# Kernel optimization log

Measured on AMD Instinct MI355X. Metric: run time of the kernel, lower is better.

The kernel has to match this reference:

```python
import jax, jax.numpy as jnp
import numpy as np

B, S, E, H, L = 16, 1024, 512, 8, 4
D = E // H  # head_dim = 64


def setup_inputs() -> dict:
    key = jax.random.key(0)
    ks = jax.random.split(key, 16)
    std = 0.02
    inp = {
        "q": jax.random.normal(ks[0], (B, S, E), jnp.float32),
        "k": jax.random.normal(ks[1], (B, S, E), jnp.float32),
        "v": jax.random.normal(ks[2], (B, S, E), jnp.float32),
        # standard Linear params (torch convention: W is (out, in))
        "Wq": jax.random.normal(ks[3], (E, E), jnp.float32) * std,
        "bq": jnp.zeros((E,), jnp.float32),
        "Wk": jax.random.normal(ks[4], (E, E), jnp.float32) * std,
        "bk": jnp.zeros((E,), jnp.float32),
        # WFLinear: shared weight elementwise-multiplied by per-language factor
        "Wv_share": jax.random.normal(ks[5], (E, E), jnp.float32) * std,
        "Wv_spec": 1.0 + jax.random.normal(ks[6], (L, E, E), jnp.float32) * std,
        "bv_share": jnp.zeros((E,), jnp.float32),
        "bv_spec": jax.random.normal(ks[7], (L, E), jnp.float32) * std,
        "Wo_share": jax.random.normal(ks[8], (E, E), jnp.float32) * std,
        "Wo_spec": 1.0 + jax.random.normal(ks[9], (L, E, E), jnp.float32) * std,
        "bo_share": jnp.zeros((E,), jnp.float32),
        "bo_spec": jax.random.normal(ks[10], (L, E), jnp.float32) * std,
        "mask": jax.random.randint(ks[11], (B, S), 0, 2, jnp.int32),
        "languageID": 1,
    }
    return inp


def reference(q, k, v, Wq, bq, Wk, bk, Wv_share, Wv_spec, bv_share, bv_spec,
              Wo_share, Wo_spec, bo_share, bo_spec, mask, languageID):
    scaling = D ** (-0.5)
    # projections (torch Linear: x @ W.T + b)
    Q = (q @ Wq.T + bq).reshape(B, S, H, D).transpose(0, 2, 1, 3) * scaling
    K = (k @ Wk.T + bk).reshape(B, S, H, D).transpose(0, 2, 1, 3)
    Wv = Wv_share * Wv_spec[languageID]
    bv = bv_share + bv_spec[languageID]
    V = (v @ Wv.T + bv).reshape(B, S, H, D).transpose(0, 2, 1, 3)
    # NOTE: faithful to original — Q already scaled by d_k^-0.5, and
    # AttentionWF divides by sqrt(d_k) AGAIN (effective scale 1/d_k).
    alpha = jnp.einsum("bhqd,bhkd->bhqk", Q, K) / np.float32(np.sqrt(D))
    m = (mask == 0)[:, None, None, :]  # (B,1,1,S) over key axis
    alpha = jnp.where(m, jnp.float32(-1e9), alpha)
    alpha = jax.nn.softmax(alpha, axis=-1)
    # dropout p=0.0 -> identity
    ctx = jnp.einsum("bhqk,bhkd->bhqd", alpha, V)  # (B,H,S,D)
    concat = ctx.transpose(0, 2, 1, 3).reshape(B, S, E)
    Wo = Wo_share * Wo_spec[languageID]
    bo = bo_share + bo_spec[languageID]
    return concat @ Wo.T + bo
```

## Files before the change

kernel.cpp:

```cpp
#include <hip/hip_runtime.h>

#define B_ 16
#define S_ 1024
#define E_ 512
#define H_ 8
#define D_ 64
#define L_ 4
#define M_ (B_*S_)

typedef unsigned short u16;
typedef __attribute__((ext_vector_type(8))) short bf16x8;
typedef __attribute__((ext_vector_type(4))) float f32x4;
typedef __attribute__((ext_vector_type(16))) float f32x16;
typedef __attribute__((ext_vector_type(4))) unsigned uint4v;
typedef __attribute__((ext_vector_type(2))) int int2v;

__device__ __forceinline__ u16 f2bf(float x) {
  unsigned u = __float_as_uint(x);
  unsigned r = (u + 0x7fffu + ((u >> 16) & 1u)) >> 16;
  return (u16)r;
}
__device__ __forceinline__ ushort4 f2bf4(float4 f) {
  ushort4 u;
  u.x = f2bf(f.x); u.y = f2bf(f.y); u.z = f2bf(f.z); u.w = f2bf(f.w);
  return u;
}
__device__ __forceinline__ unsigned cvt_pk_bf16(float lo, float hi) {
  unsigned r;
  asm("v_cvt_pk_bf16_f32 %0, %1, %2" : "=v"(r) : "v"(lo), "v"(hi));
  return r;
}
__device__ __forceinline__ int2v plswap(unsigned x, unsigned y) {
  return __builtin_amdgcn_permlane32_swap((int)x, (int)y, false, false);
}

typedef __attribute__((address_space(1))) const void gconst_void;
typedef __attribute__((address_space(3))) void lds_void;
__device__ __forceinline__ void gl_lds16(const void* g, void* l) {
  __builtin_amdgcn_global_load_lds((gconst_void*)g, (lds_void*)l, 16, 0, 0);
}
__device__ __forceinline__ void fence_vm0_barrier() {
  asm volatile("s_waitcnt vmcnt(0)" ::: "memory");
  __builtin_amdgcn_s_barrier();
}

__global__ __launch_bounds__(256) void prep_w(
    const float* __restrict__ Wq, const float* __restrict__ Wk,
    const float* __restrict__ Wv_sh, const float* __restrict__ Wv_sp,
    const float* __restrict__ Wo_sh, const float* __restrict__ Wo_sp,
    const float* __restrict__ bv_sh, const float* __restrict__ bv_sp,
    const float* __restrict__ bo_sh, const float* __restrict__ bo_sp,
    const int* __restrict__ langp,
    u16* __restrict__ Wq_b, u16* __restrict__ Wk_b,
    u16* __restrict__ Wv_b, u16* __restrict__ Wo_b,
    float* __restrict__ bv_f, float* __restrict__ bo_f) {
  int lang = langp[0];
  int i = blockIdx.x * 256 + threadIdx.x;
  size_t wofs = (size_t)lang * (E_*E_/4) + i;
  ((ushort4*)Wq_b)[i] = f2bf4(((const float4*)Wq)[i]);
  ((ushort4*)Wk_b)[i] = f2bf4(((const float4*)Wk)[i]);
  float4 vs = ((const float4*)Wv_sh)[i], vp = ((const float4*)Wv_sp)[wofs];
  float4 os = ((const float4*)Wo_sh)[i], op = ((const float4*)Wo_sp)[wofs];
  float4 vv = {vs.x*vp.x, vs.y*vp.y, vs.z*vp.z, vs.w*vp.w};
  float4 oo = {os.x*op.x, os.y*op.y, os.z*op.z, os.w*op.w};
  ((ushort4*)Wv_b)[i] = f2bf4(vv);
  ((ushort4*)Wo_b)[i] = f2bf4(oo);
  if (i < E_/4) {
    float4 b1 = ((const float4*)bv_sh)[i], b2 = ((const float4*)(bv_sp + (size_t)lang*E_))[i];
    float4 b3 = ((const float4*)bo_sh)[i], b4 = ((const float4*)(bo_sp + (size_t)lang*E_))[i];
    float4 r1 = {b1.x+b2.x, b1.y+b2.y, b1.z+b2.z, b1.w+b2.w};
    float4 r2 = {b3.x+b4.x, b3.y+b4.y, b3.z+b4.z, b3.w+b4.w};
    ((float4*)bv_f)[i] = r1;
    ((float4*)bo_f)[i] = r2;
  }
}

#define ABBUF 8192
__global__ __launch_bounds__(256, 4) void gemm_qkv(
    const float* __restrict__ q, const float* __restrict__ k, const float* __restrict__ v,
    const u16* __restrict__ Wq_b, const u16* __restrict__ Wk_b, const u16* __restrict__ Wv_b,
    const float* __restrict__ bq, const float* __restrict__ bk, const float* __restrict__ bv,
    u16* __restrict__ Qb, u16* __restrict__ Kb, u16* __restrict__ Vt) {
  __shared__ __align__(16) u16 sA[2*4096];
  __shared__ __align__(16) u16 sB[2*4096];
  const int z = blockIdx.y;
  const float* A    = (z == 0) ? q : (z == 1) ? k : v;
  const u16*   Bw   = (z == 0) ? Wq_b : (z == 1) ? Wk_b : Wv_b;
  const float* bias = (z == 0) ? bq : (z == 1) ? bk : bv;
  const int t = threadIdx.x;
  const int hw = blockIdx.x;
  const int wk = (hw & 7) * 64 + (hw >> 3);
  const int m0 = (wk >> 2) * 128, n0 = (wk & 3) * 128;
  const int lane = t & 63, wid = t >> 6;
  const int m16 = lane & 15, qq = lane >> 4;
  const int wrow = (wid >> 1) * 64, wcol = (wid & 1) * 64;
  const int key = (lane & 7) << 4;
  f32x4 acc[4][4] = {};
  const int arow = t >> 1;
  const float* aR = A + (size_t)(m0 + arow) * E_ + (t & 1) * 16;
  const int awr0 = (arow*64 + (t&1)*32)      ^ ((arow & 7) << 4);
  const int awr1 = (arow*64 + (t&1)*32 + 16) ^ ((arow & 7) << 4);
  const int cb0 = wid*2, cb1 = wid*2 + 1;
  const int rl0 = ((lane>>2)&1) ^ ((lane>>4)&1);
  const int brow = 2*(lane>>3) + rl0;
  const int bcol = (((lane&1)^rl0)<<3) + ((((lane>>1)&1) ^ ((lane>>3)&1))<<4);
  const u16* bp0 = Bw + (size_t)(n0 + cb0*16 + brow) * E_ + bcol;
  const u16* bp1 = Bw + (size_t)(n0 + cb1*16 + brow) * E_ + bcol;
  char* sAb = (char*)sA;
  char* sBb = (char*)sB;
  gl_lds16(bp0, sBb + cb0*1024);
  gl_lds16(bp1, sBb + cb1*1024);
  f32x4 ar0 = *(const f32x4*)aR;
  f32x4 ar1 = *(const f32x4*)(aR + 4);
  f32x4 ar2 = *(const f32x4*)(aR + 8);
  f32x4 ar3 = *(const f32x4*)(aR + 12);
  aR += 32; bp0 += 32; bp1 += 32;
  asm volatile("s_waitcnt vmcnt(0)" ::: "memory");
  {
    uint4v w0 = { cvt_pk_bf16(ar0[0],ar0[1]), cvt_pk_bf16(ar0[2],ar0[3]),
                  cvt_pk_bf16(ar1[0],ar1[1]), cvt_pk_bf16(ar1[2],ar1[3]) };
    uint4v w1 = { cvt_pk_bf16(ar2[0],ar2[1]), cvt_pk_bf16(ar2[2],ar2[3]),
                  cvt_pk_bf16(ar3[0],ar3[1]), cvt_pk_bf16(ar3[2],ar3[3]) };
    *(uint4v*)(sAb + awr0) = w0;
    *(uint4v*)(sAb + awr1) = w1;
  }
  asm volatile("s_waitcnt lgkmcnt(0)" ::: "memory");
  __builtin_amdgcn_s_barrier();
  for (int kt = 0; kt < 16; ++kt) {
    const int cur = (kt & 1) * ABBUF;
    const int nxt = ABBUF - cur;
    if (kt < 15) {
      gl_lds16(bp0, sBb + nxt + cb0*1024);
      gl_lds16(bp1, sBb + nxt + cb1*1024);
      ar0 = *(const f32x4*)aR;
      ar1 = *(const f32x4*)(aR + 4);
      ar2 = *(const f32x4*)(aR + 8);
      ar3 = *(const f32x4*)(aR + 12);
      aR += 32; bp0 += 32; bp1 += 32;
    }
    bf16x8 af[4], bfm[4];
#pragma unroll
    for (int mt = 0; mt < 4; ++mt) {
      int row = wrow + mt*16 + m16;
      af[mt] = *(const bf16x8*)(sAb + cur + ((row*64 + qq*16) ^ key));
    }
#pragma unroll
    for (int nt = 0; nt < 4; ++nt) {
      int row = wcol + nt*16 + m16;
      bfm[nt] = *(const bf16x8*)(sBb + cur + ((row*64 + qq*16) ^ key));
    }
#pragma unroll
    for (int mt = 0; mt < 4; ++mt)
#pragma unroll
      for (int nt = 0; nt < 4; ++nt)
        acc[mt][nt] = __builtin_amdgcn_mfma_f32_16x16x32_bf16(af[mt], bfm[nt], acc[mt][nt], 0, 0, 0);
    if (kt < 15) {
      asm volatile("s_waitcnt vmcnt(0)" ::: "memory");
      uint4v w0 = { cvt_pk_bf16(ar0[0],ar0[1]), cvt_pk_bf16(ar0[2],ar0[3]),
                    cvt_pk_bf16(ar1[0],ar1[1]), cvt_pk_bf16(ar1[2],ar1[3]) };
      uint4v w1 = { cvt_pk_bf16(ar2[0],ar2[1]), cvt_pk_bf16(ar2[2],ar2[3]),
                    cvt_pk_bf16(ar3[0],ar3[1]), cvt_pk_bf16(ar3[2],ar3[3]) };
      *(uint4v*)(sAb + nxt + awr0) = w0;
      *(uint4v*)(sAb + nxt + awr1) = w1;
      asm volatile("s_waitcnt lgkmcnt(0)" ::: "memory");
      __builtin_amdgcn_s_barrier();
    }
  }
  float bvv[4];
#pragma unroll
  for (int nt = 0; nt < 4; ++nt) bvv[nt] = bias[n0 + wcol + nt*16 + m16];
  if (z < 2) {
    u16* out = (z == 0) ? Qb : Kb;
#pragma unroll
    for (int mt = 0; mt < 4; ++mt) {
      int gm = m0 + wrow + mt*16 + qq*4;
#pragma unroll
      for (int nt = 0; nt < 4; ++nt) {
        int gn = n0 + wcol + nt*16 + m16;
#pragma unroll
        for (int r = 0; r < 4; ++r)
          out[(size_t)(gm + r) * E_ + gn] = f2bf(acc[mt][nt][r] + bvv[nt]);
      }
    }
  } else {
#pragma unroll
    for (int mt = 0; mt < 4; ++mt) {
      int tok0 = m0 + wrow + mt*16 + qq*4;
      int bb = tok0 >> 10, s0 = tok0 & 1023;
#pragma unroll
      for (int nt = 0; nt < 4; ++nt) {
        int dim = n0 + wcol + nt*16 + m16;
        uint2 wv = { cvt_pk_bf16(acc[mt][nt][0] + bvv[nt], acc[mt][nt][1] + bvv[nt]),
                     cvt_pk_bf16(acc[mt][nt][2] + bvv[nt], acc[mt][nt][3] + bvv[nt]) };
        *(uint2*)(Vt + ((size_t)(bb*E_ + dim))*S_ + s0) = wv;
      }
    }
  }
}

__global__ __launch_bounds__(256, 4) void gemm_lds(
    const u16* __restrict__ A, const u16* __restrict__ Bw,
    const float* __restrict__ bias, float* __restrict__ out) {
  __shared__ __align__(16) u16 sAD[2*4096];
  __shared__ __align__(16) u16 sBD[2*2048];
  const int t = threadIdx.x;
  const int hw = blockIdx.x;
  const int wk = (hw & 7) * 128 + (hw >> 3);
  const int m0 = (wk >> 3) * 128, n0 = (wk & 7) * 64;
  const int lane = t & 63, wid = t >> 6;
  const int m16 = lane & 15, qq = lane >> 4;
  const int wrow = (wid >> 1) * 64, wcol = (wid & 1) * 32;
  const int key = (lane & 7) << 4;
  f32x4 acc[4][2] = {};
  const int rl0 = ((lane>>2)&1) ^ ((lane>>4)&1);
  const int brow = 2*(lane>>3) + rl0;
  const int bcol = (((lane&1)^rl0)<<3) + ((((lane>>1)&1) ^ ((lane>>3)&1))<<4);
  const int c0 = 2*wid, c1 = 2*wid + 1;
  const u16* a0 = A  + (size_t)(m0 + c0*16 + brow) * E_ + bcol;
  const u16* a1 = A  + (size_t)(m0 + c1*16 + brow) * E_ + bcol;
  const u16* b0 = Bw + (size_t)(n0 + wid*16 + brow) * E_ + bcol;
  char* sAb = (char*)sAD;
  char* sBb = (char*)sBD;
  gl_lds16(a0, sAb + c0*1024);
  gl_lds16(a1, sAb + c1*1024);
  gl_lds16(b0, sBb + wid*1024);
  a0 += 32; a1 += 32; b0 += 32;
  fence_vm0_barrier();
  for (int kt = 0; kt < 16; ++kt) {
    const int curA = (kt & 1) * 8192, nxtA = 8192 - curA;
    const int curB = (kt & 1) * 4096, nxtB = 4096 - curB;
    if (kt < 15) {
      gl_lds16(a0, sAb + nxtA + c0*1024);
      gl_lds16(a1, sAb + nxtA + c1*1024);
      gl_lds16(b0, sBb + nxtB + wid*1024);
      a0 += 32; a1 += 32; b0 += 32;
    }
    bf16x8 af[4], bfm[2];
#pragma unroll
    for (int mt = 0; mt < 4; ++mt) {
      int row = wrow + mt*16 + m16;
      af[mt] = *(const bf16x8*)(sAb + curA + ((row*64 + qq*16) ^ key));
    }
#pragma unroll
    for (int nt = 0; nt < 2; ++nt) {
      int row = wcol + nt*16 + m16;
      bfm[nt] = *(const bf16x8*)(sBb + curB + ((row*64 + qq*16) ^ key));
    }
#pragma unroll
    for (int mt = 0; mt < 4; ++mt)
#pragma unroll
      for (int nt = 0; nt < 2; ++nt)
        acc[mt][nt] = __builtin_amdgcn_mfma_f32_16x16x32_bf16(af[mt], bfm[nt], acc[mt][nt], 0, 0, 0);
    if (kt < 15) fence_vm0_barrier();
  }
  float bv[2];
#pragma unroll
  for (int nt = 0; nt < 2; ++nt) bv[nt] = bias[n0 + wcol + nt*16 + m16];
#pragma unroll
  for (int mt = 0; mt < 4; ++mt) {
    int gm = m0 + wrow + mt*16 + qq*4;
#pragma unroll
    for (int nt = 0; nt < 2; ++nt) {
      int gn = n0 + wcol + nt*16 + m16;
#pragma unroll
      for (int r = 0; r < 4; ++r)
        out[(size_t)(gm + r) * E_ + gn] = acc[mt][nt][r] + bv[nt];
    }
  }
}

#define KST 72
__global__ __launch_bounds__(256) void attn_mfma(
    const u16* __restrict__ Qb, const u16* __restrict__ Kb, const u16* __restrict__ Vt,
    const int* __restrict__ mask, u16* __restrict__ ctxb) {
  __shared__ __align__(16) u16 sKV[2*64*KST];
  __shared__ __align__(16) float sMask[64];
  __shared__ __align__(16) float sL[128];
  u16* sK = sKV;
  u16* sV = sKV + 64*KST;
  const int t = threadIdx.x;
  const int lane = t & 63, w = t >> 6;
  const int l31 = lane & 31, lh = lane >> 5;
  const int hw = blockIdx.x;
  const int wk = (hw & 7) * 128 + (hw >> 3);
  const int bh = wk >> 3, b = bh >> 3, h = bh & 7;
  const int qblk = (wk & 7) * 128;
  const int q0 = qblk + w * 32;
  bf16x8 qfr[4];
  {
    const u16* qp = Qb + (size_t)(b*S_ + q0 + l31) * E_ + h*D_ + lh*8;
#pragma unroll
    for (int s = 0; s < 4; ++s) qfr[s] = *(const bf16x8*)(qp + s*16);
  }
  f32x16 oacc[2] = {};
  float lpart = 0.f;
  const int srow = t >> 2, sc0 = (t & 3) * 16;
  const u16* kp = Kb + (size_t)(b*S_ + srow) * E_ + h*D_ + sc0;
  const u16* vp = Vt + ((size_t)(b*H_ + h) * D_ + srow) * S_ + sc0;
  uint4 rk0 = *(const uint4*)kp, rk1 = *(const uint4*)(kp + 8);
  uint4 rv0 = *(const uint4*)vp, rv1 = *(const uint4*)(vp + 8);
  float rmsk = 0.f;
  if (t < 64) rmsk = (mask[b*S_ + t] == 0) ? -1e9f : 0.f;
  const float CS = 0.015625f * 1.44269504f;
  for (int kt = 0; kt < S_; kt += 64) {
    *(uint4*)&sK[srow*KST + sc0]     = rk0;
    *(uint4*)&sK[srow*KST + sc0 + 8] = rk1;
    *(uint4*)&sV[srow*KST + sc0]     = rv0;
    *(uint4*)&sV[srow*KST + sc0 + 8] = rv1;
    if (t < 64) sMask[t] = rmsk;
    __syncthreads();
    if (kt + 64 < S_) {
      kp += (size_t)64 * E_; vp += 64;
      rk0 = *(const uint4*)kp; rk1 = *(const uint4*)(kp + 8);
      rv0 = *(const uint4*)vp; rv1 = *(const uint4*)(vp + 8);
      if (t < 64) rmsk = (mask[b*S_ + kt + 64 + t] == 0) ? -1e9f : 0.f;
    }
    f32x16 sacc[2] = {};
#pragma unroll
    for (int mt = 0; mt < 2; ++mt)
#pragma unroll
      for (int s = 0; s < 4; ++s) {
        bf16x8 kf = *(const bf16x8*)&sK[(mt*32 + l31)*KST + s*16 + lh*8];
        sacc[mt] = __builtin_amdgcn_mfma_f32_32x32x16_bf16(kf, qfr[s], sacc[mt], 0, 0, 0);
      }
    unsigned pw[2][4][2];
#pragma unroll
    for (int mt = 0; mt < 2; ++mt)
#pragma unroll
      for (int g = 0; g < 4; ++g) {
        f32x4 msk = *(const f32x4*)&sMask[mt*32 + g*8 + lh*4];
        float p0 = exp2f(fmaf(sacc[mt][4*g+0], CS, msk[0]));
        float p1 = exp2f(fmaf(sacc[mt][4*g+1], CS, msk[1]));
        float p2 = exp2f(fmaf(sacc[mt][4*g+2], CS, msk[2]));
        float p3 = exp2f(fmaf(sacc[mt][4*g+3], CS, msk[3]));
        lpart += (p0 + p1) + (p2 + p3);
        pw[mt][g][0] = cvt_pk_bf16(p0, p1);
        pw[mt][g][1] = cvt_pk_bf16(p2, p3);
      }
#pragma unroll
    for (int s = 0; s < 4; ++s) {
      const int mt = s >> 1, c = s & 1;
      int2v P1 = plswap(pw[mt][2*c][0], pw[mt][2*c+1][0]);
      int2v P2 = plswap(pw[mt][2*c][1], pw[mt][2*c+1][1]);
      union { uint4v u; bf16x8 h8; } pa;
      pa.u = (uint4v){ (unsigned)P1[0], (unsigned)P2[0], (unsigned)P1[1], (unsigned)P2[1] };
#pragma unroll
      for (int nt = 0; nt < 2; ++nt) {
        bf16x8 vf = *(const bf16x8*)&sV[(nt*32 + l31)*KST + s*16 + lh*8];
        oacc[nt] = __builtin_amdgcn_mfma_f32_32x32x16_bf16(pa.h8, vf, oacc[nt], 0, 0, 0);
      }
    }
    __syncthreads();
  }
  lpart += __shfl_xor(lpart, 32);
  if (lane < 32) sL[w*32 + l31] = lpart;
  f32x4 linv[4];
#pragma unroll
  for (int g = 0; g < 4; ++g) {
    f32x4 lv = *(const f32x4*)&sL[w*32 + 8*g + 4*lh];
    linv[g] = (f32x4){1.0f/lv[0], 1.0f/lv[1], 1.0f/lv[2], 1.0f/lv[3]};
  }
#pragma unroll
  for (int nt = 0; nt < 2; ++nt)
#pragma unroll
    for (int g = 0; g < 4; ++g)
#pragma unroll
      for (int r2 = 0; r2 < 4; ++r2) {
        int qoff = 8*g + 4*lh + r2;
        sKV[(w*32 + qoff)*KST + nt*32 + l31] = f2bf(oacc[nt][4*g+r2] * linv[g][r2]);
      }
  __syncthreads();
  const int row = t >> 1, c0 = (t & 1) * 32;
  uint4 o0 = *(uint4*)&sKV[row*KST + c0];
  uint4 o1 = *(uint4*)&sKV[row*KST + c0 + 8];
  uint4 o2 = *(uint4*)&sKV[row*KST + c0 + 16];
  uint4 o3 = *(uint4*)&sKV[row*KST + c0 + 24];
  u16* dst = ctxb + (size_t)(b*S_ + qblk + row) * E_ + h*D_ + c0;
  *(uint4*)dst = o0;
  *(uint4*)(dst + 8)  = o1;
  *(uint4*)(dst + 16) = o2;
  *(uint4*)(dst + 24) = o3;
}

extern "C" void kernel_launch(void* const* d_in, const int* in_sizes, int n_in,
                              void* d_out, int out_size, void* d_ws, size_t ws_size,
                              hipStream_t stream) {
  const float* q     = (const float*)d_in[0];
  const float* k     = (const float*)d_in[1];
  const float* v     = (const float*)d_in[2];
  const float* Wq    = (const float*)d_in[3];
  const float* bq    = (const float*)d_in[4];
  const float* Wk    = (const float*)d_in[5];
  const float* bk    = (const float*)d_in[6];
  const float* Wv_sh = (const float*)d_in[7];
  const float* Wv_sp = (const float*)d_in[8];
  const float* bv_sh = (const float*)d_in[9];
  const float* bv_sp = (const float*)d_in[10];
  const float* Wo_sh = (const float*)d_in[11];
  const float* Wo_sp = (const float*)d_in[12];
  const float* bo_sh = (const float*)d_in[13];
  const float* bo_sp = (const float*)d_in[14];
  const int*   mask  = (const int*)d_in[15];
  const int*   lang  = (const int*)d_in[16];

  char* ws = (char*)d_ws;
  size_t off = 0;
  auto alloc = [&](size_t bytes) -> char* {
    char* p = ws + off;
    off += (bytes + 255) & ~(size_t)255;
    return p;
  };
  u16* Qb   = (u16*)alloc((size_t)M_ * E_ * 2);
  u16* Kb   = (u16*)alloc((size_t)M_ * E_ * 2);
  u16* Vt   = (u16*)alloc((size_t)M_ * E_ * 2);
  u16* ctxb = (u16*)alloc((size_t)M_ * E_ * 2);
  u16* Wq_b = (u16*)alloc((size_t)E_ * E_ * 2);
  u16* Wk_b = (u16*)alloc((size_t)E_ * E_ * 2);
  u16* Wv_b = (u16*)alloc((size_t)E_ * E_ * 2);
  u16* Wo_b = (u16*)alloc((size_t)E_ * E_ * 2);
  float* bv_f = (float*)alloc(E_ * 4);
  float* bo_f = (float*)alloc(E_ * 4);

  prep_w<<<E_*E_/1024, 256, 0, stream>>>(Wq, Wk, Wv_sh, Wv_sp, Wo_sh, Wo_sp,
                                         bv_sh, bv_sp, bo_sh, bo_sp, lang,
                                         Wq_b, Wk_b, Wv_b, Wo_b, bv_f, bo_f);

  dim3 qkvgrid(512, 3);
  gemm_qkv<<<qkvgrid, 256, 0, stream>>>(q, k, v, Wq_b, Wk_b, Wv_b,
                                        bq, bk, bv_f, Qb, Kb, Vt);

  attn_mfma<<<1024, 256, 0, stream>>>(Qb, Kb, Vt, mask, ctxb);

  gemm_lds<<<1024, 256, 0, stream>>>(ctxb, Wo_b, bo_f, (float*)d_out);
}
```

Before: 301.8 us.

## Deepen GEMM pipelines to four-stage LDS ring with partial vmcnt waits

Both projection GEMMs move from double buffering with full vmcnt(0) drains to a four-slot LDS ring that prefetches three k-tiles ahead. Waits use partial vmcnt counts, and the QKV kernel holds three tiles of fp32 A in registers. MFMA blocks are wrapped in s_setprio to favour math issue. The aim is to hide global-load latency; the costs are more LDS and registers, which cut occupancy from 4 to 3 blocks, plus a fully unrolled loop.

```diff
diff --git a/kernel.cpp b/kernel.cpp
--- a/kernel.cpp
+++ b/kernel.cpp
@@ -38,10 +38,6 @@
 typedef __attribute__((address_space(3))) void lds_void;
 __device__ __forceinline__ void gl_lds16(const void* g, void* l) {
   __builtin_amdgcn_global_load_lds((gconst_void*)g, (lds_void*)l, 16, 0, 0);
-}
-__device__ __forceinline__ void fence_vm0_barrier() {
-  asm volatile("s_waitcnt vmcnt(0)" ::: "memory");
-  __builtin_amdgcn_s_barrier();
 }
 
 __global__ __launch_bounds__(256) void prep_w(
@@ -75,14 +71,13 @@
   }
 }
 
-#define ABBUF 8192
-__global__ __launch_bounds__(256, 4) void gemm_qkv(
+__global__ __launch_bounds__(256, 3) void gemm_qkv(
     const float* __restrict__ q, const float* __restrict__ k, const float* __restrict__ v,
     const u16* __restrict__ Wq_b, const u16* __restrict__ Wk_b, const u16* __restrict__ Wv_b,
     const float* __restrict__ bq, const float* __restrict__ bk, const float* __restrict__ bv,
     u16* __restrict__ Qb, u16* __restrict__ Kb, u16* __restrict__ Vt) {
   __shared__ __align__(16) u16 sA[2*4096];
-  __shared__ __align__(16) u16 sB[2*4096];
+  __shared__ __align__(16) u16 sB[4*4096];
   const int z = blockIdx.y;
   const float* A    = (z == 0) ? q : (z == 1) ? k : v;
   const u16*   Bw   = (z == 0) ? Wq_b : (z == 1) ? Wk_b : Wv_b;
@@ -100,6 +95,7 @@
   const float* aR = A + (size_t)(m0 + arow) * E_ + (t & 1) * 16;
   const int awr0 = (arow*64 + (t&1)*32)      ^ ((arow & 7) << 4);
   const int awr1 = (arow*64 + (t&1)*32 + 16) ^ ((arow & 7) << 4);
+  f32x4 rA[3][4];
   const int cb0 = wid*2, cb1 = wid*2 + 1;
   const int rl0 = ((lane>>2)&1) ^ ((lane>>4)&1);
   const int brow = 2*(lane>>3) + rl0;
@@ -108,63 +104,59 @@
   const u16* bp1 = Bw + (size_t)(n0 + cb1*16 + brow) * E_ + bcol;
   char* sAb = (char*)sA;
   char* sBb = (char*)sB;
-  gl_lds16(bp0, sBb + cb0*1024);
-  gl_lds16(bp1, sBb + cb1*1024);
-  f32x4 ar0 = *(const f32x4*)aR;
-  f32x4 ar1 = *(const f32x4*)(aR + 4);
-  f32x4 ar2 = *(const f32x4*)(aR + 8);
-  f32x4 ar3 = *(const f32x4*)(aR + 12);
-  aR += 32; bp0 += 32; bp1 += 32;
-  asm volatile("s_waitcnt vmcnt(0)" ::: "memory");
-  {
-    uint4v w0 = { cvt_pk_bf16(ar0[0],ar0[1]), cvt_pk_bf16(ar0[2],ar0[3]),
-                  cvt_pk_bf16(ar1[0],ar1[1]), cvt_pk_bf16(ar1[2],ar1[3]) };
-    uint4v w1 = { cvt_pk_bf16(ar2[0],ar2[1]), cvt_pk_bf16(ar2[2],ar2[3]),
-                  cvt_pk_bf16(ar3[0],ar3[1]), cvt_pk_bf16(ar3[2],ar3[3]) };
-    *(uint4v*)(sAb + awr0) = w0;
-    *(uint4v*)(sAb + awr1) = w1;
-  }
-  asm volatile("s_waitcnt lgkmcnt(0)" ::: "memory");
-  __builtin_amdgcn_s_barrier();
+#pragma unroll
+  for (int p = 0; p < 3; ++p) {
+    gl_lds16(bp0, sBb + p*8192 + cb0*1024);
+    gl_lds16(bp1, sBb + p*8192 + cb1*1024);
+    rA[p][0] = *(const f32x4*)aR;
+    rA[p][1] = *(const f32x4*)(aR + 4);
+    rA[p][2] = *(const f32x4*)(aR + 8);
+    rA[p][3] = *(const f32x4*)(aR + 12);
+    aR += 32; bp0 += 32; bp1 += 32;
+  }
+#pragma unroll
   for (int kt = 0; kt < 16; ++kt) {
-    const int cur = (kt & 1) * ABBUF;
-    const int nxt = ABBUF - cur;
-    if (kt < 15) {
-      gl_lds16(bp0, sBb + nxt + cb0*1024);
-      gl_lds16(bp1, sBb + nxt + cb1*1024);
-      ar0 = *(const f32x4*)aR;
-      ar1 = *(const f32x4*)(aR + 4);
-      ar2 = *(const f32x4*)(aR + 8);
-      ar3 = *(const f32x4*)(aR + 12);
+    if (kt < 14)       asm volatile("s_waitcnt vmcnt(12)" ::: "memory");
+    else if (kt == 14) asm volatile("s_waitcnt vmcnt(6)" ::: "memory");
+    else               asm volatile("s_waitcnt vmcnt(0)" ::: "memory");
+    {
+      f32x4 a0 = rA[kt%3][0], a1 = rA[kt%3][1], a2 = rA[kt%3][2], a3 = rA[kt%3][3];
+      uint4v w0 = { cvt_pk_bf16(a0[0],a0[1]), cvt_pk_bf16(a0[2],a0[3]),
+                    cvt_pk_bf16(a1[0],a1[1]), cvt_pk_bf16(a1[2],a1[3]) };
+      uint4v w1 = { cvt_pk_bf16(a2[0],a2[1]), cvt_pk_bf16(a2[2],a2[3]),
+                    cvt_pk_bf16(a3[0],a3[1]), cvt_pk_bf16(a3[2],a3[3]) };
+      *(uint4v*)(sAb + (kt&1)*8192 + awr0) = w0;
+      *(uint4v*)(sAb + (kt&1)*8192 + awr1) = w1;
+    }
+    asm volatile("s_waitcnt lgkmcnt(0)" ::: "memory");
+    __builtin_amdgcn_s_barrier();
+    if (kt < 13) {
+      gl_lds16(bp0, sBb + ((kt+3)&3)*8192 + cb0*1024);
+      gl_lds16(bp1, sBb + ((kt+3)&3)*8192 + cb1*1024);
+      rA[(kt+3)%3][0] = *(const f32x4*)aR;
+      rA[(kt+3)%3][1] = *(const f32x4*)(aR + 4);
+      rA[(kt+3)%3][2] = *(const f32x4*)(aR + 8);
+      rA[(kt+3)%3][3] = *(const f32x4*)(aR + 12);
       aR += 32; bp0 += 32; bp1 += 32;
     }
     bf16x8 af[4], bfm[4];
 #pragma unroll
     for (int mt = 0; mt < 4; ++mt) {
       int row = wrow + mt*16 + m16;
-      af[mt] = *(const bf16x8*)(sAb + cur + ((row*64 + qq*16) ^ key));
+      af[mt] = *(const bf16x8*)(sAb + (kt&1)*8192 + ((row*64 + qq*16) ^ key));
     }
 #pragma unroll
     for (int nt = 0; nt < 4; ++nt) {
       int row = wcol + nt*16 + m16;
-      bfm[nt] = *(const bf16x8*)(sBb + cur + ((row*64 + qq*16) ^ key));
-    }
+      bfm[nt] = *(const bf16x8*)(sBb + (kt&3)*8192 + ((row*64 + qq*16) ^ key));
+    }
+    __builtin_amdgcn_s_setprio(1);
 #pragma unroll
     for (int mt = 0; mt < 4; ++mt)
 #pragma unroll
       for (int nt = 0; nt < 4; ++nt)
         acc[mt][nt] = __builtin_amdgcn_mfma_f32_16x16x32_bf16(af[mt], bfm[nt], acc[mt][nt], 0, 0, 0);
-    if (kt < 15) {
-      asm volatile("s_waitcnt vmcnt(0)" ::: "memory");
-      uint4v w0 = { cvt_pk_bf16(ar0[0],ar0[1]), cvt_pk_bf16(ar0[2],ar0[3]),
-                    cvt_pk_bf16(ar1[0],ar1[1]), cvt_pk_bf16(ar1[2],ar1[3]) };
-      uint4v w1 = { cvt_pk_bf16(ar2[0],ar2[1]), cvt_pk_bf16(ar2[2],ar2[3]),
-                    cvt_pk_bf16(ar3[0],ar3[1]), cvt_pk_bf16(ar3[2],ar3[3]) };
-      *(uint4v*)(sAb + nxt + awr0) = w0;
-      *(uint4v*)(sAb + nxt + awr1) = w1;
-      asm volatile("s_waitcnt lgkmcnt(0)" ::: "memory");
-      __builtin_amdgcn_s_barrier();
-    }
+    __builtin_amdgcn_s_setprio(0);
   }
   float bvv[4];
 #pragma unroll
@@ -198,11 +190,11 @@
   }
 }
 
-__global__ __launch_bounds__(256, 4) void gemm_lds(
+__global__ __launch_bounds__(256, 3) void gemm_lds(
     const u16* __restrict__ A, const u16* __restrict__ Bw,
     const float* __restrict__ bias, float* __restrict__ out) {
-  __shared__ __align__(16) u16 sAD[2*4096];
-  __shared__ __align__(16) u16 sBD[2*2048];
+  __shared__ __align__(16) u16 sAD[4*4096];
+  __shared__ __align__(16) u16 sBD[4*2048];
   const int t = threadIdx.x;
   const int hw = blockIdx.x;
   const int wk = (hw & 7) * 128 + (hw >> 3);
@@ -221,37 +213,43 @@
   const u16* b0 = Bw + (size_t)(n0 + wid*16 + brow) * E_ + bcol;
   char* sAb = (char*)sAD;
   char* sBb = (char*)sBD;
-  gl_lds16(a0, sAb + c0*1024);
-  gl_lds16(a1, sAb + c1*1024);
-  gl_lds16(b0, sBb + wid*1024);
-  a0 += 32; a1 += 32; b0 += 32;
-  fence_vm0_barrier();
+#pragma unroll
+  for (int p = 0; p < 3; ++p) {
+    gl_lds16(a0, sAb + p*8192 + c0*1024);
+    gl_lds16(a1, sAb + p*8192 + c1*1024);
+    gl_lds16(b0, sBb + p*4096 + wid*1024);
+    a0 += 32; a1 += 32; b0 += 32;
+  }
+#pragma unroll
   for (int kt = 0; kt < 16; ++kt) {
-    const int curA = (kt & 1) * 8192, nxtA = 8192 - curA;
-    const int curB = (kt & 1) * 4096, nxtB = 4096 - curB;
-    if (kt < 15) {
-      gl_lds16(a0, sAb + nxtA + c0*1024);
-      gl_lds16(a1, sAb + nxtA + c1*1024);
-      gl_lds16(b0, sBb + nxtB + wid*1024);
+    if (kt < 14)       asm volatile("s_waitcnt vmcnt(6)" ::: "memory");
+    else if (kt == 14) asm volatile("s_waitcnt vmcnt(3)" ::: "memory");
+    else               asm volatile("s_waitcnt vmcnt(0)" ::: "memory");
+    __builtin_amdgcn_s_barrier();
+    if (kt < 13) {
+      gl_lds16(a0, sAb + ((kt+3)&3)*8192 + c0*1024);
+      gl_lds16(a1, sAb + ((kt+3)&3)*8192 + c1*1024);
+      gl_lds16(b0, sBb + ((kt+3)&3)*4096 + wid*1024);
       a0 += 32; a1 += 32; b0 += 32;
     }
     bf16x8 af[4], bfm[2];
 #pragma unroll
     for (int mt = 0; mt < 4; ++mt) {
       int row = wrow + mt*16 + m16;
-      af[mt] = *(const bf16x8*)(sAb + curA + ((row*64 + qq*16) ^ key));
+      af[mt] = *(const bf16x8*)(sAb + (kt&3)*8192 + ((row*64 + qq*16) ^ key));
     }
 #pragma unroll
     for (int nt = 0; nt < 2; ++nt) {
       int row = wcol + nt*16 + m16;
-      bfm[nt] = *(const bf16x8*)(sBb + curB + ((row*64 + qq*16) ^ key));
-    }
+      bfm[nt] = *(const bf16x8*)(sBb + (kt&3)*4096 + ((row*64 + qq*16) ^ key));
+    }
+    __builtin_amdgcn_s_setprio(1);
 #pragma unroll
     for (int mt = 0; mt < 4; ++mt)
 #pragma unroll
       for (int nt = 0; nt < 2; ++nt)
         acc[mt][nt] = __builtin_amdgcn_mfma_f32_16x16x32_bf16(af[mt], bfm[nt], acc[mt][nt], 0, 0, 0);
-    if (kt < 15) fence_vm0_barrier();
+    __builtin_amdgcn_s_setprio(0);
   }
   float bv[2];
 #pragma unroll
```

New measurement: 305.6 us. Within noise of the previous version (+1.3%).
